# Kernel optimization log

Measured on AMD Instinct MI355X. Metric: run time of the kernel, lower is better.

## Reference

```python
import jax, jax.numpy as jnp
import numpy as np

PRUNE_N, PRUNE_M = 2, 4
RIA_A = 1.0
NUM_HEADS = 16
HEAD_DIM = 128
ROPE_THETA = 10000.0


def sparse_mask(W, scaler_row, perm):
    # RIA metric: |W|/colsum + |W|/rowsum, scaled by sqrt(scaler_row)**a
    absW = jnp.abs(W)
    metric = (absW / absW.sum(axis=0, keepdims=True)
              + absW / absW.sum(axis=1, keepdims=True))
    metric = metric * (jnp.sqrt(scaler_row)[None, :] ** RIA_A)
    Wm = metric @ perm                      # permute columns: [R, C]
    R, C = Wm.shape
    nb = C // PRUNE_M
    blocks = Wm.reshape(R, nb, PRUNE_M)
    # hard N:M mask: top-n per block of m
    _, idx = jax.lax.top_k(blocks, PRUNE_N)           # [R, nb, n]
    hard = jax.nn.one_hot(idx, PRUNE_M, dtype=Wm.dtype).sum(axis=-2)  # [R, nb, m]
    soft = jax.nn.softmax(blocks, axis=-1)
    hard = hard.reshape(R, C) @ perm.T
    soft = soft.reshape(R, C) @ perm.T
    # straight-through estimator
    return jax.lax.stop_gradient(hard - soft) + soft


def sparse_linear(x, W, b, scaler_row, perm):
    Wm = W * sparse_mask(W, scaler_row, perm)
    y = jnp.einsum('bsh,oh->bso', x, Wm)
    return y + b if b is not None else y


def rotate_half(x):
    x1, x2 = jnp.split(x, 2, axis=-1)
    return jnp.concatenate([-x2, x1], axis=-1)


def rope_tables(seq_len, dim, dtype):
    inv_freq = 1.0 / (ROPE_THETA ** (jnp.arange(0, dim, 2, dtype=jnp.float32) / dim))
    t = jnp.arange(seq_len, dtype=jnp.float32)
    freqs = jnp.outer(t, inv_freq)               # [S, dim/2]
    emb = jnp.concatenate([freqs, freqs], axis=-1)  # [S, dim]
    return jnp.cos(emb).astype(dtype), jnp.sin(emb).astype(dtype)


def setup_inputs() -> dict:
    key = jax.random.key(0)
    ks = jax.random.split(key, 16)
    H = 2048
    B, S = 2, 2048
    inp = {
        'hidden_states': jax.random.normal(ks[0], (B, S, H), jnp.float32) * 0.02,
        'Wq': jax.random.normal(ks[1], (H, H), jnp.float32) * 0.02,
        'bq': jax.random.normal(ks[2], (H,), jnp.float32) * 0.02,
        'Wk': jax.random.normal(ks[3], (H, H), jnp.float32) * 0.02,
        'bk': jax.random.normal(ks[4], (H,), jnp.float32) * 0.02,
        'Wv': jax.random.normal(ks[5], (H, H), jnp.float32) * 0.02,
        'bv': jax.random.normal(ks[6], (H,), jnp.float32) * 0.02,
        'Wo': jax.random.normal(ks[7], (H, H), jnp.float32) * 0.02,
        'sq': jax.random.uniform(ks[8], (H,), jnp.float32, 0.1, 1.0),
        'sk': jax.random.uniform(ks[9], (H,), jnp.float32, 0.1, 1.0),
        'sv': jax.random.uniform(ks[10], (H,), jnp.float32, 0.1, 1.0),
        'so': jax.random.uniform(ks[11], (H,), jnp.float32, 0.1, 1.0),
        'perm_qkv': jax.random.normal(ks[12], (H, H), jnp.float32) * 0.02,
        'perm_o': jax.random.normal(ks[13], (H, H), jnp.float32) * 0.02,
        'position_ids': jnp.broadcast_to(jnp.arange(S, dtype=jnp.int64), (B, S)),
    }
    return inp


def reference(hidden_states, Wq, bq, Wk, bk, Wv, bv, Wo,
              sq, sk, sv, so, perm_qkv, perm_o, position_ids):
    B, S, H = hidden_states.shape
    q = sparse_linear(hidden_states, Wq, bq, sq, perm_qkv)
    k = sparse_linear(hidden_states, Wk, bk, sk, perm_qkv)
    v = sparse_linear(hidden_states, Wv, bv, sv, perm_qkv)

    q = q.reshape(B, S, NUM_HEADS, HEAD_DIM).transpose(0, 2, 1, 3)  # [B,Hh,S,D]
    k = k.reshape(B, S, NUM_HEADS, HEAD_DIM).transpose(0, 2, 1, 3)
    v = v.reshape(B, S, NUM_HEADS, HEAD_DIM).transpose(0, 2, 1, 3)

    cos, sin = rope_tables(S, HEAD_DIM, q.dtype)
    c = cos[position_ids][:, None]  # [B,1,S,D]
    s = sin[position_ids][:, None]
    q = q * c + rotate_half(q) * s
    k = k * c + rotate_half(k) * s

    scores = jnp.einsum('bhqd,bhkd->bhqk', q, k) / np.sqrt(HEAD_DIM)
    causal = jnp.tril(jnp.ones((S, S), dtype=bool))
    scores = jnp.where(causal[None, None], scores, jnp.finfo(jnp.float32).min)
    attn = jax.nn.softmax(scores.astype(jnp.float32), axis=-1).astype(q.dtype)
    out = jnp.einsum('bhqk,bhkd->bhqd', attn, v)
    out = out.transpose(0, 2, 1, 3).reshape(B, S, H)
    out = sparse_linear(out, Wo, None, so, perm_o)
    return out
```

## Files before the change

kernel.cpp:

```cpp
#include <hip/hip_runtime.h>
#include <cstdint>
#include <cstddef>

typedef __attribute__((ext_vector_type(4))) float  f32x4;
typedef __attribute__((ext_vector_type(4))) int    i32x4;
typedef __attribute__((ext_vector_type(8))) short  s16x8;
typedef __attribute__((ext_vector_type(4))) short  s16x4;
typedef __attribute__((ext_vector_type(8))) __bf16 bf16x8;

struct Ptr4 { const float* p[4]; };

#define DEV __device__ __forceinline__

DEV unsigned short f2bf_u(float x) {
  unsigned u = __builtin_bit_cast(unsigned, x);
  u += 0x7fffu + ((u >> 16) & 1u);
  return (unsigned short)(u >> 16);
}
DEV float bfu2f(unsigned short u) {
  return __builtin_bit_cast(float, ((unsigned)u) << 16);
}
DEV bf16x8 ld_frag(const unsigned short* p) {
  s16x8 v = *(const s16x8*)p;
  return __builtin_bit_cast(bf16x8, v);
}
DEV f32x4 mfma16(bf16x8 a, bf16x8 b, f32x4 c) {
  return __builtin_amdgcn_mfma_f32_16x16x32_bf16(a, b, c, 0, 0, 0);
}
DEV void gload_lds16(const unsigned short* g, unsigned short* l) {
  __builtin_amdgcn_global_load_lds(
      (const __attribute__((address_space(1))) unsigned int*)g,
      (__attribute__((address_space(3))) unsigned int*)l, 16, 0, 0);
}
DEV int xcd_swizzle(int bid, int nwg) {
  const int q8 = nwg >> 3;
  return (bid & 7) * q8 + (bid >> 3);
}

__global__ __launch_bounds__(256)
void k_rowsum(Ptr4 Ws, float* __restrict__ rowsums)
{
  const int row = blockIdx.x, mat = blockIdx.y, tid = threadIdx.x;
  const float* W = Ws.p[mat] + (size_t)row * 2048;
  float s = 0.f;
  #pragma unroll
  for (int p = 0; p < 2; ++p) {
    f32x4 v = *(const f32x4*)(W + p * 1024 + tid * 4);
    s += fabsf(v[0]) + fabsf(v[1]) + fabsf(v[2]) + fabsf(v[3]);
  }
  #pragma unroll
  for (int off = 1; off < 64; off <<= 1) s += __shfl_xor(s, off);
  __shared__ float red[4];
  if ((tid & 63) == 0) red[tid >> 6] = s;
  __syncthreads();
  if (tid == 0) rowsums[mat * 2048 + row] = red[0] + red[1] + red[2] + red[3];
}

__global__ __launch_bounds__(256)
void k_colsum_part(Ptr4 Ws, float* __restrict__ part)
{
  const int c = blockIdx.x * 256 + threadIdx.x;
  const int r0 = blockIdx.y * 64;
  const int mat = blockIdx.z;
  const float* W = Ws.p[mat];
  float s = 0.f;
  for (int rr = 0; rr < 64; ++rr) s += fabsf(W[(size_t)(r0 + rr) * 2048 + c]);
  part[((size_t)mat * 32 + blockIdx.y) * 2048 + c] = s;
}
__global__ __launch_bounds__(256)
void k_colsum_red(const float* __restrict__ part, float* __restrict__ colsums)
{
  const int gid = blockIdx.x * 256 + threadIdx.x;
  const int mat = gid >> 11, c = gid & 2047;
  float s = 0.f;
  #pragma unroll
  for (int j = 0; j < 32; ++j) s += part[((size_t)mat * 32 + j) * 2048 + c];
  colsums[gid] = s;
}

__global__ __launch_bounds__(256)
void k_metric(Ptr4 Ws, Ptr4 Ss, const float* __restrict__ rowsums,
              const float* __restrict__ colsums,
              unsigned short* __restrict__ mhi, unsigned short* __restrict__ mlo)
{
  const size_t idx4 = ((size_t)blockIdx.x * 256 + threadIdx.x) * 4;
  const int row = (int)(idx4 >> 11);
  const int c = (int)(idx4 & 2047);
  const int mat = row >> 11, rl = row & 2047;
  const float rs = rowsums[mat * 2048 + rl];
  f32x4 w  = *(const f32x4*)(Ws.p[mat] + (size_t)rl * 2048 + c);
  f32x4 cs = *(const f32x4*)(colsums + mat * 2048 + c);
  f32x4 sv = *(const f32x4*)(Ss.p[mat] + c);
  s16x4 hv, lv;
  #pragma unroll
  for (int j = 0; j < 4; ++j) {
    const float a = fabsf(w[j]);
    const float m = (a / cs[j] + a / rs) * sqrtf(sv[j]);
    const unsigned short hb = f2bf_u(m);
    hv[j] = (short)hb;
    lv[j] = (short)f2bf_u(m - bfu2f(hb));
  }
  *(s16x4*)(mhi + idx4) = hv;
  *(s16x4*)(mlo + idx4) = lv;
}

__global__ __launch_bounds__(256)
void k_perm_prep(const float* __restrict__ pq, const float* __restrict__ po,
                 unsigned short* __restrict__ thi_q, unsigned short* __restrict__ tlo_q,
                 unsigned short* __restrict__ thi_o, unsigned short* __restrict__ tlo_o,
                 unsigned short* __restrict__ pb_q, unsigned short* __restrict__ pb_o)
{
  __shared__ float T[64 * 65];
  const int which = blockIdx.z;
  const float* src = which ? po : pq;
  unsigned short* thi = which ? thi_o : thi_q;
  unsigned short* tlo = which ? tlo_o : tlo_q;
  unsigned short* pb  = which ? pb_o : pb_q;
  const int rb = blockIdx.y * 64, cb = blockIdx.x * 64, tid = threadIdx.x;
  #pragma unroll
  for (int i = 0; i < 4; ++i) {
    const int cc = i * 256 + tid;
    const int rowl = cc >> 4, c4 = (cc & 15) * 4;
    f32x4 v = *(const f32x4*)(src + (size_t)(rb + rowl) * 2048 + cb + c4);
    s16x4 pc;
    #pragma unroll
    for (int j = 0; j < 4; ++j) {
      T[rowl * 65 + c4 + j] = v[j];
      pc[j] = (short)f2bf_u(v[j]);
    }
    *(s16x4*)(pb + (size_t)(rb + rowl) * 2048 + cb + c4) = pc;
  }
  __syncthreads();
  #pragma unroll
  for (int i = 0; i < 4; ++i) {
    const int cc = i * 256 + tid;
    const int rowt = cc >> 4, c4 = (cc & 15) * 4;
    s16x4 hh, ll;
    #pragma unroll
    for (int j = 0; j < 4; ++j) {
      const float v = T[(c4 + j) * 65 + rowt];
      const unsigned short hb = f2bf_u(v);
      hh[j] = (short)hb;
      ll[j] = (short)f2bf_u(v - bfu2f(hb));
    }
    const size_t off = (size_t)(cb + rowt) * 2048 + rb + c4;
    *(s16x4*)(thi + off) = hh;
    *(s16x4*)(tlo + off) = ll;
  }
}

__global__ __launch_bounds__(256)
void k_cast_bf(const float* __restrict__ src, unsigned short* __restrict__ dst)
{
  const size_t i = ((size_t)blockIdx.x * 256 + threadIdx.x) * 8;
  f32x4 a = *(const f32x4*)(src + i);
  f32x4 b = *(const f32x4*)(src + i + 4);
  s16x8 o;
  #pragma unroll
  for (int j = 0; j < 4; ++j) o[j] = (short)f2bf_u(a[j]);
  #pragma unroll
  for (int j = 0; j < 4; ++j) o[4 + j] = (short)f2bf_u(b[j]);
  *(s16x8*)(dst + i) = o;
}

__global__ __launch_bounds__(256)
void k_rope_tab(float* __restrict__ ct, float* __restrict__ st)
{
  const int gid = blockIdx.x * 256 + threadIdx.x;
  const int s = gid >> 6, i = gid & 63;
  const float ex = (float)(2 * i) / 128.f;
  const float inv = 1.f / powf(10000.f, ex);
  const float f = (float)s * inv;
  ct[gid] = cosf(f);
  st[gid] = sinf(f);
}

__global__ __launch_bounds__(256)
void k_rope_reshape(const unsigned short* __restrict__ yqkv, const int* __restrict__ pos,
                    const float* __restrict__ ct, const float* __restrict__ st,
                    unsigned short* __restrict__ qo, unsigned short* __restrict__ ko)
{
  const int gid = blockIdx.x * 256 + threadIdx.x;
  const int d8 = gid & 15;
  const int s = (gid >> 4) & 2047;
  const int h = (gid >> 15) & 15;
  const int b = gid >> 19;
  const int t = b * 2048 + s;
  const int p = pos[t];
  const size_t yb = (size_t)t * 6144 + h * 128;
  s16x8 qv = *(const s16x8*)(yqkv + yb + d8 * 8);
  s16x8 qp = *(const s16x8*)(yqkv + yb + (d8 ^ 8) * 8);
  s16x8 kv = *(const s16x8*)(yqkv + yb + 2048 + d8 * 8);
  s16x8 kp = *(const s16x8*)(yqkv + yb + 2048 + (d8 ^ 8) * 8);
  const int dh0 = (d8 & 7) * 8;
  const float sgn = (d8 < 8) ? -1.f : 1.f;
  s16x8 qo8, ko8;
  #pragma unroll
  for (int j = 0; j < 8; ++j) {
    const float cv = ct[p * 64 + dh0 + j];
    const float sv = st[p * 64 + dh0 + j];
    const float q0 = bfu2f((unsigned short)qv[j]);
    const float k0 = bfu2f((unsigned short)kv[j]);
    const float q1 = sgn * bfu2f((unsigned short)qp[j]);
    const float k1 = sgn * bfu2f((unsigned short)kp[j]);
    qo8[j] = (short)f2bf_u(q0 * cv + q1 * sv);
    ko8[j] = (short)f2bf_u(k0 * cv + k1 * sv);
  }
  const size_t o = ((size_t)(b * 16 + h) * 2048 + s) * 128 + d8 * 8;
  *(s16x8*)(qo + o) = qo8;
  *(s16x8*)(ko + o) = ko8;
}

__global__ __launch_bounds__(256)
void k_vtrans(const unsigned short* __restrict__ yqkv, unsigned short* __restrict__ vt)
{
  __shared__ float T[64 * 129];
  const int st = blockIdx.x, bh = blockIdx.y, tid = threadIdx.x;
  const int b = bh >> 4, h = bh & 15;
  #pragma unroll
  for (int i = 0; i < 4; ++i) {
    const int c = i * 256 + tid;
    const int sl = c >> 4, d8 = (c & 15) * 8;
    s16x8 v = *(const s16x8*)(yqkv + (size_t)(b * 2048 + st * 64 + sl) * 6144 + 4096 + h * 128 + d8);
    #pragma unroll
    for (int j = 0; j < 8; ++j) T[sl * 129 + d8 + j] = bfu2f((unsigned short)v[j]);
  }
  __syncthreads();
  #pragma unroll
  for (int i = 0; i < 4; ++i) {
    const int c = i * 256 + tid;
    const int d = c >> 3, s8 = (c & 7) * 8;
    s16x8 o;
    #pragma unroll
    for (int j = 0; j < 8; ++j) o[j] = (short)f2bf_u(T[(s8 + j) * 129 + d]);
    *(s16x8*)(vt + ((size_t)bh * 128 + d) * 2048 + st * 64 + s8) = o;
  }
}

template<int MODE, int SPLIT, int SWZ>
__global__ __launch_bounds__(256)
void gemm_bt(const unsigned short* __restrict__ Ahi, const unsigned short* __restrict__ Alo,
             const unsigned short* __restrict__ Bhi_1, const unsigned short* __restrict__ Blo_1,
             const unsigned short* __restrict__ Bhi_2, const unsigned short* __restrict__ Blo_2,
             int bswitch,
             float* __restrict__ Cf, unsigned short* __restrict__ Cb,
             Ptr4 aux, int M, int N, int K)
{
  __shared__ alignas(16) unsigned short As[2 * 4096];
  __shared__ alignas(16) unsigned short Bs[2 * 4096];
  const int tid = threadIdx.x;
  const int lane = tid & 63, wid = tid >> 6;
  const int wm = wid >> 1, wn = wid & 1;
  const int r = lane & 15, g = lane >> 4;
  int bx = blockIdx.x, by = blockIdx.y;
  if (SWZ) {
    const int nwg = gridDim.x * gridDim.y;
    const int sw = xcd_swizzle(blockIdx.y * gridDim.x + blockIdx.x, nwg);
    bx = sw % gridDim.x; by = sw / gridDim.x;
  }
  const int mbase = by * 128;
  const int nbase = bx * 128;
  const int KT = K >> 5;
  (void)M;
  const unsigned short* Bhi = (mbase >= bswitch) ? Bhi_2 : Bhi_1;
  const unsigned short* Blo = (mbase >= bswitch) ? Blo_2 : Blo_1;

  const f32x4 zero = {0.f, 0.f, 0.f, 0.f};
  f32x4 acc[4][4];
  #pragma unroll
  for (int i = 0; i < 4; ++i) {
    #pragma unroll
    for (int j = 0; j < 4; ++j) acc[i][j] = zero;
  }

  const int srl = lane >> 2;
  const int sch = lane & 3;

  auto issue_tile = [&](int kt, int buf) {
    const size_t kb = (size_t)kt * 32;
    #pragma unroll
    for (int i = 0; i < 2; ++i) {
      const int rbase = wid * 32 + i * 16;
      const int rloc = rbase + srl;
      const int sc = ((sch ^ ((rloc >> 1) & 3)) << 3);
      const size_t ga = (size_t)(mbase + rloc) * K + kb + sc;
      const size_t gb = (size_t)(nbase + rloc) * K + kb + sc;
      gload_lds16(Ahi + ga, &As[buf * 4096 + rbase * 32]);
      gload_lds16(Bhi + gb, &Bs[buf * 4096 + rbase * 32]);
      if (SPLIT) {
        gload_lds16(Alo + ga, &As[4096 + rbase * 32]);
        gload_lds16(Blo + gb, &Bs[4096 + rbase * 32]);
      }
    }
  };

  if (SPLIT) {
    issue_tile(0, 0);
    for (int kt = 0; kt < KT; ++kt) {
      __syncthreads();

      bf16x8 ah[4], bfr[4], al[4], bl[4];
      #pragma unroll
      for (int mi = 0; mi < 4; ++mi) {
        const int arow = wm * 64 + mi * 16 + r;
        const int sw2 = ((g ^ ((arow >> 1) & 3)) << 3);
        ah[mi] = ld_frag(&As[arow * 32 + sw2]);
        al[mi] = ld_frag(&As[4096 + arow * 32 + sw2]);
      }
      #pragma unroll
      for (int ni = 0; ni < 4; ++ni) {
        const int brow = wn * 64 + ni * 16 + r;
        const int sw2 = ((g ^ ((brow >> 1) & 3)) << 3);
        bfr[ni] = ld_frag(&Bs[brow * 32 + sw2]);
        bl[ni] = ld_frag(&Bs[4096 + brow * 32 + sw2]);
      }
      __syncthreads();
      if (kt + 1 < KT) issue_tile(kt + 1, 0);

      #pragma unroll
      for (int mi = 0; mi < 4; ++mi) {
        #pragma unroll
        for (int ni = 0; ni < 4; ++ni) {
          acc[mi][ni] = mfma16(al[mi], bfr[ni], acc[mi][ni]);
          acc[mi][ni] = mfma16(ah[mi], bl[ni], acc[mi][ni]);
          acc[mi][ni] = mfma16(ah[mi], bfr[ni], acc[mi][ni]);
        }
      }
    }
  } else {
    issue_tile(0, 0);
    int cur = 0;
    for (int kt = 0; kt < KT; ++kt) {
      __syncthreads();
      if (kt + 1 < KT) issue_tile(kt + 1, cur ^ 1);

      bf16x8 ah[4], bfr[4];
      #pragma unroll
      for (int mi = 0; mi < 4; ++mi) {
        const int arow = wm * 64 + mi * 16 + r;
        ah[mi] = ld_frag(&As[cur * 4096 + arow * 32 + ((g ^ ((arow >> 1) & 3)) << 3)]);
      }
      #pragma unroll
      for (int ni = 0; ni < 4; ++ni) {
        const int brow = wn * 64 + ni * 16 + r;
        bfr[ni] = ld_frag(&Bs[cur * 4096 + brow * 32 + ((g ^ ((brow >> 1) & 3)) << 3)]);
      }
      #pragma unroll
      for (int mi = 0; mi < 4; ++mi) {
        #pragma unroll
        for (int ni = 0; ni < 4; ++ni)
          acc[mi][ni] = mfma16(ah[mi], bfr[ni], acc[mi][ni]);
      }
      cur ^= 1;
    }
  }

  #pragma unroll
  for (int mi = 0; mi < 4; ++mi) {
    #pragma unroll
    for (int ni = 0; ni < 4; ++ni) {
      const int row0 = mbase + wm * 64 + mi * 16 + g * 4;
      const int col  = nbase + wn * 64 + ni * 16 + r;
      if (MODE == 0) {
        #pragma unroll
        for (int e = 0; e < 4; ++e)
          Cf[(size_t)(row0 + e) * N + col] = acc[mi][ni][e];
      } else if (MODE == 1) {
        const float* wsrc = aux.p[row0 >> 11];
        #pragma unroll
        for (int e = 0; e < 4; ++e) {
          const float mval = wsrc[(size_t)((row0 + e) & 2047) * 2048 + col];
          Cb[(size_t)(row0 + e) * N + col] = f2bf_u(acc[mi][ni][e] * mval);
        }
      } else if (MODE == 2) {
        const float* bp = aux.p[col >> 11];
        const float bb = bp[col & 2047];
        #pragma unroll
        for (int e = 0; e < 4; ++e)
          Cb[(size_t)(row0 + e) * N + col] = f2bf_u(acc[mi][ni][e] + bb);
      } else {
        const int ii = r & 3;
        #pragma unroll
        for (int e = 0; e < 4; ++e) {
          const float v  = acc[mi][ni][e];
          const float v1 = __shfl_xor(v, 1);
          const float v2 = __shfl_xor(v, 2);
          const float v3 = __shfl_xor(v, 3);
          int cnt = 0;
          { const int j = ii ^ 1; cnt += (v1 > v) || (v1 == v && j < ii); }
          { const int j = ii ^ 2; cnt += (v2 > v) || (v2 == v && j < ii); }
          { const int j = ii ^ 3; cnt += (v3 > v) || (v3 == v && j < ii); }
          Cb[(size_t)(row0 + e) * N + col] =
              (cnt < 2) ? (unsigned short)0x3F80 : (unsigned short)0;
        }
      }
    }
  }
}

__global__ __launch_bounds__(256)
void attn_fa(const unsigned short* __restrict__ Qh, const unsigned short* __restrict__ Kh,
             const unsigned short* __restrict__ Vt, unsigned short* __restrict__ Out)
{
  __shared__ alignas(16) unsigned short Ks[64 * 128];
  __shared__ alignas(16) unsigned short Vs[128 * 64];
  __shared__ alignas(16) unsigned short Ps[4][1024];
  const int tid = threadIdx.x, lane = tid & 63, wid = tid >> 6;
  const int r = lane & 15, g = lane >> 4;
  const int sw = xcd_swizzle(blockIdx.y * gridDim.x + blockIdx.x, gridDim.x * gridDim.y);
  const int pair = sw % 16, bh = sw / 16;
  const int b = bh >> 4, h = bh & 15;
  const f32x4 zero = {0.f, 0.f, 0.f, 0.f};

  i32x4 kr[4], vr[4];
  auto issue_kv = [&](int kvt) {
    #pragma unroll
    for (int i = 0; i < 4; ++i) {
      const int c = i * 256 + tid;
      {
        const int row = c >> 4, slot = c & 15;
        kr[i] = *(const i32x4*)(Kh + ((size_t)bh * 2048 + kvt * 64 + row) * 128 + slot * 8);
      }
      {
        const int row = c >> 3, slot = c & 7;
        vr[i] = *(const i32x4*)(Vt + ((size_t)bh * 128 + row) * 2048 + kvt * 64 + slot * 8);
      }
    }
  };

  for (int half = 0; half < 2; ++half) {
    const int qt = half ? (31 - pair) : pair;
    const int qrow0 = qt * 64 + wid * 16;

    bf16x8 qf[4];
    {
      const unsigned short* qp = Qh + ((size_t)bh * 2048 + qrow0 + r) * 128;
      #pragma unroll
      for (int ks = 0; ks < 4; ++ks) qf[ks] = ld_frag(qp + ks * 32 + g * 8);
    }
    f32x4 oacc[8];
    #pragma unroll
    for (int i = 0; i < 8; ++i) oacc[i] = zero;
    float m_run[4] = {-1e30f, -1e30f, -1e30f, -1e30f};
    float l_run[4] = {0.f, 0.f, 0.f, 0.f};

    issue_kv(0);
    for (int kvt = 0; kvt <= qt; ++kvt) {
      __syncthreads();
      #pragma unroll
      for (int i = 0; i < 4; ++i) {
        const int c = i * 256 + tid;
        {
          const int row = c >> 4, slot = c & 15;
          *(i32x4*)&Ks[row * 128 + ((slot ^ (row & 7)) << 3)] = kr[i];
        }
        {
          const int row = c >> 3, slot = c & 7;
          *(i32x4*)&Vs[row * 64 + ((slot ^ (row & 7)) << 3)] = vr[i];
        }
      }
      __syncthreads();
      if (kvt < qt) issue_kv(kvt + 1);

      f32x4 sc[4];
      #pragma unroll
      for (int ni = 0; ni < 4; ++ni) sc[ni] = zero;
      __builtin_amdgcn_s_setprio(1);
      #pragma unroll
      for (int ks = 0; ks < 4; ++ks) {
        const int slot = (ks << 2) | g;
        #pragma unroll
        for (int ni = 0; ni < 4; ++ni) {
          const int krow = ni * 16 + r;
          bf16x8 kf = ld_frag(&Ks[krow * 128 + ((slot ^ (krow & 7)) << 3)]);
          sc[ni] = mfma16(qf[ks], kf, sc[ni]);
        }
      }
      __builtin_amdgcn_s_setprio(0);
      const float sscale = 0.08838834764831845f;
      if (kvt == qt) {
        #pragma unroll
        for (int ni = 0; ni < 4; ++ni) {
          const int kvg = kvt * 64 + ni * 16 + r;
          #pragma unroll
          for (int e = 0; e < 4; ++e) {
            const int qg = qrow0 + g * 4 + e;
            const float s = sc[ni][e] * sscale;
            sc[ni][e] = (kvg > qg) ? -1e30f : s;
          }
        }
      } else {
        #pragma unroll
        for (int ni = 0; ni < 4; ++ni) {
          #pragma unroll
          for (int e = 0; e < 4; ++e) sc[ni][e] *= sscale;
        }
      }
      float corr[4];
      #pragma unroll
      for (int e = 0; e < 4; ++e) {
        float mx = fmaxf(fmaxf(sc[0][e], sc[1][e]), fmaxf(sc[2][e], sc[3][e]));
        mx = fmaxf(mx, __shfl_xor(mx, 1));
        mx = fmaxf(mx, __shfl_xor(mx, 2));
        mx = fmaxf(mx, __shfl_xor(mx, 4));
        mx = fmaxf(mx, __shfl_xor(mx, 8));
        const float mn = fmaxf(m_run[e], mx);
        corr[e] = exp2f((m_run[e] - mn) * 1.4426950408889634f);
        m_run[e] = mn;
      }
      float psum[4] = {0.f, 0.f, 0.f, 0.f};
      #pragma unroll
      for (int ni = 0; ni < 4; ++ni) {
        #pragma unroll
        for (int e = 0; e < 4; ++e) {
          const float p = exp2f((sc[ni][e] - m_run[e]) * 1.4426950408889634f);
          sc[ni][e] = p;
          psum[e] += p;
        }
      }
      #pragma unroll
      for (int e = 0; e < 4; ++e) {
        float s = psum[e];
        s += __shfl_xor(s, 1);
        s += __shfl_xor(s, 2);
        s += __shfl_xor(s, 4);
        s += __shfl_xor(s, 8);
        l_run[e] = l_run[e] * corr[e] + s;
      }
      #pragma unroll
      for (int nf = 0; nf < 8; ++nf) {
        #pragma unroll
        for (int e = 0; e < 4; ++e) oacc[nf][e] *= corr[e];
      }
      #pragma unroll
      for (int ni = 0; ni < 4; ++ni) {
        #pragma unroll
        for (int e = 0; e < 4; ++e) {
          const int prow = g * 4 + e;
          const int col = ni * 16 + r;
          const int slot = col >> 3;
          Ps[wid][prow * 64 + ((slot ^ (prow & 7)) << 3) + (col & 7)] = f2bf_u(sc[ni][e]);
        }
      }
      __builtin_amdgcn_s_setprio(1);
      #pragma unroll
      for (int ks = 0; ks < 2; ++ks) {
        const int slot = (ks << 2) | g;
        bf16x8 pf = ld_frag(&Ps[wid][r * 64 + ((slot ^ (r & 7)) << 3)]);
        #pragma unroll
        for (int nf = 0; nf < 8; ++nf) {
          const int vrow = nf * 16 + r;
          bf16x8 vf = ld_frag(&Vs[vrow * 64 + ((slot ^ (vrow & 7)) << 3)]);
          oacc[nf] = mfma16(pf, vf, oacc[nf]);
        }
      }
      __builtin_amdgcn_s_setprio(0);
    }
    #pragma unroll
    for (int e = 0; e < 4; ++e) {
      const float inv = 1.f / l_run[e];
      const int qg = qrow0 + g * 4 + e;
      #pragma unroll
      for (int nf = 0; nf < 8; ++nf) {
        const int d = nf * 16 + r;
        Out[((size_t)(b * 2048 + qg)) * 2048 + h * 128 + d] = f2bf_u(oacc[nf][e] * inv);
      }
    }
  }
}

extern "C" void kernel_launch(void* const* d_in, const int* in_sizes, int n_in,
                              void* d_out, int out_size, void* d_ws, size_t ws_size,
                              hipStream_t stream)
{
  (void)in_sizes; (void)n_in; (void)out_size; (void)ws_size;
  const float* hid   = (const float*)d_in[0];
  const float* Wq    = (const float*)d_in[1];
  const float* bq    = (const float*)d_in[2];
  const float* Wk    = (const float*)d_in[3];
  const float* bk    = (const float*)d_in[4];
  const float* Wv    = (const float*)d_in[5];
  const float* bv    = (const float*)d_in[6];
  const float* Wo    = (const float*)d_in[7];
  const float* sq    = (const float*)d_in[8];
  const float* sk    = (const float*)d_in[9];
  const float* sv    = (const float*)d_in[10];
  const float* so    = (const float*)d_in[11];
  const float* permq = (const float*)d_in[12];
  const float* permo = (const float*)d_in[13];
  const int* pos     = (const int*)d_in[14];
  float* out = (float*)d_out;
  char* ws = (char*)d_ws;

  constexpr size_t OFF_ROWS = 0;
  constexpr size_t OFF_COLS = OFF_ROWS + (size_t)4 * 2048 * 4;
  constexpr size_t OFF_PART = OFF_COLS + (size_t)4 * 2048 * 4;
  constexpr size_t OFF_COS  = OFF_PART + (size_t)4 * 32 * 2048 * 4;
  constexpr size_t OFF_SIN  = OFF_COS + (size_t)2048 * 64 * 4;
  constexpr size_t SZ_PERM  = (size_t)2048 * 2048 * 2;
  constexpr size_t OFF_A    = OFF_SIN + (size_t)2048 * 64 * 4;
  constexpr size_t OFF_PTQH = OFF_A;
  constexpr size_t OFF_PTQL = OFF_PTQH + SZ_PERM;
  constexpr size_t OFF_PTOH = OFF_PTQL + SZ_PERM;
  constexpr size_t OFF_PTOL = OFF_PTOH + SZ_PERM;
  constexpr size_t OFF_PBQ  = OFF_PTOL + SZ_PERM;
  constexpr size_t OFF_PBO  = OFF_PBQ + SZ_PERM;
  constexpr size_t SZ_M8    = (size_t)8192 * 2048 * 2;
  constexpr size_t OFF_B    = OFF_PBO + SZ_PERM;
  constexpr size_t OFF_C    = OFF_B + SZ_M8;
  constexpr size_t OFF_D    = OFF_C + SZ_M8;
  constexpr size_t OFF_E    = OFF_D + SZ_M8;

  float* rowsums = (float*)(ws + OFF_ROWS);
  float* colsums = (float*)(ws + OFF_COLS);
  float* part    = (float*)(ws + OFF_PART);
  float* cost    = (float*)(ws + OFF_COS);
  float* sint    = (float*)(ws + OFF_SIN);
  unsigned short* ptqh = (unsigned short*)(ws + OFF_PTQH);
  unsigned short* ptql = (unsigned short*)(ws + OFF_PTQL);
  unsigned short* ptoh = (unsigned short*)(ws + OFF_PTOH);
  unsigned short* ptol = (unsigned short*)(ws + OFF_PTOL);
  unsigned short* pbq  = (unsigned short*)(ws + OFF_PBQ);
  unsigned short* pbo  = (unsigned short*)(ws + OFF_PBO);
  unsigned short* mhi  = (unsigned short*)(ws + OFF_B);
  unsigned short* mlo  = (unsigned short*)(ws + OFF_C);
  unsigned short* hard = (unsigned short*)(ws + OFF_D);
  unsigned short* wfin = (unsigned short*)(ws + OFF_E);
  unsigned short* yqkv = (unsigned short*)(ws + OFF_B);
  unsigned short* qhb  = (unsigned short*)(ws + OFF_A);
  unsigned short* khb  = (unsigned short*)(ws + OFF_A + 2 * SZ_PERM);
  unsigned short* vtg  = (unsigned short*)(ws + OFF_A + 4 * SZ_PERM);
  unsigned short* xbf  = (unsigned short*)(ws + OFF_D);
  unsigned short* att  = (unsigned short*)(ws + OFF_D + SZ_M8 / 2);

  Ptr4 Wptrs{{Wq, Wk, Wv, Wo}};
  Ptr4 Sptrs{{sq, sk, sv, so}};
  Ptr4 BiasP{{bq, bk, bv, nullptr}};
  Ptr4 NoAux{{nullptr, nullptr, nullptr, nullptr}};
  constexpr int NOSW = 1 << 30;

  k_rowsum<<<dim3(2048, 4), 256, 0, stream>>>(Wptrs, rowsums);
  k_colsum_part<<<dim3(8, 32, 4), 256, 0, stream>>>(Wptrs, part);
  k_colsum_red<<<32, 256, 0, stream>>>(part, colsums);
  k_metric<<<16384, 256, 0, stream>>>(Wptrs, Sptrs, rowsums, colsums, mhi, mlo);
  k_perm_prep<<<dim3(32, 32, 2), 256, 0, stream>>>(permq, permo, ptqh, ptql, ptoh, ptol, pbq, pbo);
  gemm_bt<3, 1, 0><<<dim3(16, 64), 256, 0, stream>>>(mhi, mlo, ptqh, ptql, ptoh, ptol, 6144,
                                                     nullptr, hard, NoAux, 8192, 2048, 2048);
  gemm_bt<1, 0, 1><<<dim3(16, 64), 256, 0, stream>>>(hard, nullptr, pbq, nullptr, pbo, nullptr, 6144,
                                                     nullptr, wfin, Wptrs, 8192, 2048, 2048);
  k_cast_bf<<<4096, 256, 0, stream>>>(hid, xbf);
  gemm_bt<2, 0, 1><<<dim3(48, 32), 256, 0, stream>>>(xbf, nullptr, wfin, nullptr, wfin, nullptr, NOSW,
                                                     nullptr, yqkv, BiasP, 4096, 6144, 2048);
  k_rope_tab<<<512, 256, 0, stream>>>(cost, sint);
  k_rope_reshape<<<4096, 256, 0, stream>>>(yqkv, pos, cost, sint, qhb, khb);
  k_vtrans<<<dim3(32, 32), 256, 0, stream>>>(yqkv, vtg);
  attn_fa<<<dim3(16, 32), 256, 0, stream>>>(qhb, khb, vtg, att);
  gemm_bt<0, 0, 1><<<dim3(16, 32), 256, 0, stream>>>(att, nullptr, wfin + (size_t)6144 * 2048, nullptr,
                                                     wfin + (size_t)6144 * 2048, nullptr, NOSW,
                                                     out, nullptr, NoAux, 4096, 2048, 2048);
}
```

Before: 648.6 us.

## Deepen split-precision GEMM K tile to 64 and halve rope loads

```diff
diff --git a/kernel.cpp b/kernel.cpp
--- a/kernel.cpp
+++ b/kernel.cpp
@@ -181,34 +181,37 @@
                     unsigned short* __restrict__ qo, unsigned short* __restrict__ ko)
 {
   const int gid = blockIdx.x * 256 + threadIdx.x;
-  const int d8 = gid & 15;
-  const int s = (gid >> 4) & 2047;
-  const int h = (gid >> 15) & 15;
-  const int b = gid >> 19;
+  const int d8p = gid & 7;
+  const int s = (gid >> 3) & 2047;
+  const int h = (gid >> 14) & 15;
+  const int b = gid >> 18;
   const int t = b * 2048 + s;
   const int p = pos[t];
   const size_t yb = (size_t)t * 6144 + h * 128;
-  s16x8 qv = *(const s16x8*)(yqkv + yb + d8 * 8);
-  s16x8 qp = *(const s16x8*)(yqkv + yb + (d8 ^ 8) * 8);
-  s16x8 kv = *(const s16x8*)(yqkv + yb + 2048 + d8 * 8);
-  s16x8 kp = *(const s16x8*)(yqkv + yb + 2048 + (d8 ^ 8) * 8);
-  const int dh0 = (d8 & 7) * 8;
-  const float sgn = (d8 < 8) ? -1.f : 1.f;
-  s16x8 qo8, ko8;
+  s16x8 qa = *(const s16x8*)(yqkv + yb + d8p * 8);
+  s16x8 qb = *(const s16x8*)(yqkv + yb + (d8p + 8) * 8);
+  s16x8 ka = *(const s16x8*)(yqkv + yb + 2048 + d8p * 8);
+  s16x8 kb = *(const s16x8*)(yqkv + yb + 2048 + (d8p + 8) * 8);
+  const int dh0 = d8p * 8;
+  s16x8 qoa, qob, koa, kob;
   #pragma unroll
   for (int j = 0; j < 8; ++j) {
     const float cv = ct[p * 64 + dh0 + j];
     const float sv = st[p * 64 + dh0 + j];
-    const float q0 = bfu2f((unsigned short)qv[j]);
-    const float k0 = bfu2f((unsigned short)kv[j]);
-    const float q1 = sgn * bfu2f((unsigned short)qp[j]);
-    const float k1 = sgn * bfu2f((unsigned short)kp[j]);
-    qo8[j] = (short)f2bf_u(q0 * cv + q1 * sv);
-    ko8[j] = (short)f2bf_u(k0 * cv + k1 * sv);
-  }
-  const size_t o = ((size_t)(b * 16 + h) * 2048 + s) * 128 + d8 * 8;
-  *(s16x8*)(qo + o) = qo8;
-  *(s16x8*)(ko + o) = ko8;
+    const float qav = bfu2f((unsigned short)qa[j]);
+    const float qbv = bfu2f((unsigned short)qb[j]);
+    const float kav = bfu2f((unsigned short)ka[j]);
+    const float kbv = bfu2f((unsigned short)kb[j]);
+    qoa[j] = (short)f2bf_u(qav * cv + (-1.f * qbv) * sv);
+    koa[j] = (short)f2bf_u(kav * cv + (-1.f * kbv) * sv);
+    qob[j] = (short)f2bf_u(qbv * cv + qav * sv);
+    kob[j] = (short)f2bf_u(kbv * cv + kav * sv);
+  }
+  const size_t o = ((size_t)(b * 16 + h) * 2048 + s) * 128 + d8p * 8;
+  *(s16x8*)(qo + o) = qoa;
+  *(s16x8*)(qo + o + 64) = qob;
+  *(s16x8*)(ko + o) = koa;
+  *(s16x8*)(ko + o + 64) = kob;
 }
 
 __global__ __launch_bounds__(256)
@@ -246,8 +249,8 @@
              float* __restrict__ Cf, unsigned short* __restrict__ Cb,
              Ptr4 aux, int M, int N, int K)
 {
-  __shared__ alignas(16) unsigned short As[2 * 4096];
-  __shared__ alignas(16) unsigned short Bs[2 * 4096];
+  __shared__ alignas(16) unsigned short As[(SPLIT ? 4 : 2) * 4096];
+  __shared__ alignas(16) unsigned short Bs[(SPLIT ? 4 : 2) * 4096];
   const int tid = threadIdx.x;
   const int lane = tid & 63, wid = tid >> 6;
   const int wm = wid >> 1, wn = wid & 1;
@@ -260,7 +263,6 @@
   }
   const int mbase = by * 128;
   const int nbase = bx * 128;
-  const int KT = K >> 5;
   (void)M;
   const unsigned short* Bhi = (mbase >= bswitch) ? Bhi_2 : Bhi_1;
   const unsigned short* Blo = (mbase >= bswitch) ? Blo_2 : Blo_1;
@@ -273,50 +275,41 @@
     for (int j = 0; j < 4; ++j) acc[i][j] = zero;
   }
 
-  const int srl = lane >> 2;
-  const int sch = lane & 3;
-
-  auto issue_tile = [&](int kt, int buf) {
-    const size_t kb = (size_t)kt * 32;
-    #pragma unroll
-    for (int i = 0; i < 2; ++i) {
-      const int rbase = wid * 32 + i * 16;
-      const int rloc = rbase + srl;
-      const int sc = ((sch ^ ((rloc >> 1) & 3)) << 3);
-      const size_t ga = (size_t)(mbase + rloc) * K + kb + sc;
-      const size_t gb = (size_t)(nbase + rloc) * K + kb + sc;
-      gload_lds16(Ahi + ga, &As[buf * 4096 + rbase * 32]);
-      gload_lds16(Bhi + gb, &Bs[buf * 4096 + rbase * 32]);
-      if (SPLIT) {
-        gload_lds16(Alo + ga, &As[4096 + rbase * 32]);
-        gload_lds16(Blo + gb, &Bs[4096 + rbase * 32]);
-      }
-    }
-  };
-
   if (SPLIT) {
-    issue_tile(0, 0);
-    for (int kt = 0; kt < KT; ++kt) {
-      __syncthreads();
-
-      bf16x8 ah[4], bfr[4], al[4], bl[4];
+    const int KT = K >> 6;
+    const int srl = lane >> 3;
+    const int sch = lane & 7;
+    auto issue_tile = [&](int kt) {
+      const size_t kb = (size_t)kt * 64;
+      #pragma unroll
+      for (int i = 0; i < 4; ++i) {
+        const int rbase = wid * 32 + i * 8;
+        const int rloc = rbase + srl;
+        const int cs = (sch ^ srl) * 8;
+        const size_t ga = (size_t)(mbase + rloc) * K + kb + cs;
+        const size_t gb = (size_t)(nbase + rloc) * K + kb + cs;
+        gload_lds16(Ahi + ga, &As[rbase * 64]);
+        gload_lds16(Alo + ga, &As[8192 + rbase * 64]);
+        gload_lds16(Bhi + gb, &Bs[rbase * 64]);
+        gload_lds16(Blo + gb, &Bs[8192 + rbase * 64]);
+      }
+    };
+    auto do_slice = [&](int ks) {
+      bf16x8 ah[4], al[4], bfr[4], bl[4];
       #pragma unroll
       for (int mi = 0; mi < 4; ++mi) {
         const int arow = wm * 64 + mi * 16 + r;
-        const int sw2 = ((g ^ ((arow >> 1) & 3)) << 3);
-        ah[mi] = ld_frag(&As[arow * 32 + sw2]);
-        al[mi] = ld_frag(&As[4096 + arow * 32 + sw2]);
+        const int co = (((ks * 4 + g) ^ (arow & 7)) << 3);
+        ah[mi] = ld_frag(&As[arow * 64 + co]);
+        al[mi] = ld_frag(&As[8192 + arow * 64 + co]);
       }
       #pragma unroll
       for (int ni = 0; ni < 4; ++ni) {
         const int brow = wn * 64 + ni * 16 + r;
-        const int sw2 = ((g ^ ((brow >> 1) & 3)) << 3);
-        bfr[ni] = ld_frag(&Bs[brow * 32 + sw2]);
-        bl[ni] = ld_frag(&Bs[4096 + brow * 32 + sw2]);
-      }
-      __syncthreads();
-      if (kt + 1 < KT) issue_tile(kt + 1, 0);
-
+        const int co = (((ks * 4 + g) ^ (brow & 7)) << 3);
+        bfr[ni] = ld_frag(&Bs[brow * 64 + co]);
+        bl[ni] = ld_frag(&Bs[8192 + brow * 64 + co]);
+      }
       #pragma unroll
       for (int mi = 0; mi < 4; ++mi) {
         #pragma unroll
@@ -326,14 +319,87 @@
           acc[mi][ni] = mfma16(ah[mi], bfr[ni], acc[mi][ni]);
         }
       }
-    }
+    };
+
+    issue_tile(0);
+    for (int kt = 0; kt < KT; ++kt) {
+      __syncthreads();
+      bf16x8 ah1[4], al1[4], bfr1[4], bl1[4];
+      {
+        bf16x8 ah[4], al[4], bfr[4], bl[4];
+        #pragma unroll
+        for (int mi = 0; mi < 4; ++mi) {
+          const int arow = wm * 64 + mi * 16 + r;
+          const int co = ((g ^ (arow & 7)) << 3);
+          ah[mi] = ld_frag(&As[arow * 64 + co]);
+          al[mi] = ld_frag(&As[8192 + arow * 64 + co]);
+        }
+        #pragma unroll
+        for (int ni = 0; ni < 4; ++ni) {
+          const int brow = wn * 64 + ni * 16 + r;
+          const int co = ((g ^ (brow & 7)) << 3);
+          bfr[ni] = ld_frag(&Bs[brow * 64 + co]);
+          bl[ni] = ld_frag(&Bs[8192 + brow * 64 + co]);
+        }
+        #pragma unroll
+        for (int mi = 0; mi < 4; ++mi) {
+          #pragma unroll
+          for (int ni = 0; ni < 4; ++ni) {
+            acc[mi][ni] = mfma16(al[mi], bfr[ni], acc[mi][ni]);
+            acc[mi][ni] = mfma16(ah[mi], bl[ni], acc[mi][ni]);
+            acc[mi][ni] = mfma16(ah[mi], bfr[ni], acc[mi][ni]);
+          }
+        }
+      }
+      #pragma unroll
+      for (int mi = 0; mi < 4; ++mi) {
+        const int arow = wm * 64 + mi * 16 + r;
+        const int co = (((4 + g) ^ (arow & 7)) << 3);
+        ah1[mi] = ld_frag(&As[arow * 64 + co]);
+        al1[mi] = ld_frag(&As[8192 + arow * 64 + co]);
+      }
+      #pragma unroll
+      for (int ni = 0; ni < 4; ++ni) {
+        const int brow = wn * 64 + ni * 16 + r;
+        const int co = (((4 + g) ^ (brow & 7)) << 3);
+        bfr1[ni] = ld_frag(&Bs[brow * 64 + co]);
+        bl1[ni] = ld_frag(&Bs[8192 + brow * 64 + co]);
+      }
+      __syncthreads();
+      if (kt + 1 < KT) issue_tile(kt + 1);
+      #pragma unroll
+      for (int mi = 0; mi < 4; ++mi) {
+        #pragma unroll
+        for (int ni = 0; ni < 4; ++ni) {
+          acc[mi][ni] = mfma16(al1[mi], bfr1[ni], acc[mi][ni]);
+          acc[mi][ni] = mfma16(ah1[mi], bl1[ni], acc[mi][ni]);
+          acc[mi][ni] = mfma16(ah1[mi], bfr1[ni], acc[mi][ni]);
+        }
+      }
+    }
+    (void)do_slice;
   } else {
+    const int KT = K >> 5;
+    const int srl = lane >> 2;
+    const int sch = lane & 3;
+    auto issue_tile = [&](int kt, int buf) {
+      const size_t kb = (size_t)kt * 32;
+      #pragma unroll
+      for (int i = 0; i < 2; ++i) {
+        const int rbase = wid * 32 + i * 16;
+        const int rloc = rbase + srl;
+        const int sc = ((sch ^ ((rloc >> 1) & 3)) << 3);
+        const size_t ga = (size_t)(mbase + rloc) * K + kb + sc;
+        const size_t gb = (size_t)(nbase + rloc) * K + kb + sc;
+        gload_lds16(Ahi + ga, &As[buf * 4096 + rbase * 32]);
+        gload_lds16(Bhi + gb, &Bs[buf * 4096 + rbase * 32]);
+      }
+    };
     issue_tile(0, 0);
     int cur = 0;
     for (int kt = 0; kt < KT; ++kt) {
       __syncthreads();
       if (kt + 1 < KT) issue_tile(kt + 1, cur ^ 1);
-
       bf16x8 ah[4], bfr[4];
       #pragma unroll
       for (int mi = 0; mi < 4; ++mi) {
@@ -652,7 +718,7 @@
   gemm_bt<2, 0, 1><<<dim3(48, 32), 256, 0, stream>>>(xbf, nullptr, wfin, nullptr, wfin, nullptr, NOSW,
                                                      nullptr, yqkv, BiasP, 4096, 6144, 2048);
   k_rope_tab<<<512, 256, 0, stream>>>(cost, sint);
-  k_rope_reshape<<<4096, 256, 0, stream>>>(yqkv, pos, cost, sint, qhb, khb);
+  k_rope_reshape<<<2048, 256, 0, stream>>>(yqkv, pos, cost, sint, qhb, khb);
   k_vtrans<<<dim3(32, 32), 256, 0, stream>>>(yqkv, vtg);
   attn_fa<<<dim3(16, 32), 256, 0, stream>>>(qhb, khb, vtg, att);
   gemm_bt<0, 0, 1><<<dim3(16, 32), 256, 0, stream>>>(att, nullptr, wfin + (size_t)6144 * 2048, nullptr,
```

Result: no change. 637.5 us (-1.7%).
